# Performance work log

Measured on AMD Instinct MI355X. Metric: run time of the kernel, lower is better.

## Reference

```python
import jax, jax.numpy as jnp
import numpy as np

TOP_K = 32
NUM_RBF = 16
D_MIN, D_MAX = 2.0, 22.0
MAX_REL = 32  # max_relative_feature

# atom index order: N=0, Ca=1, C=2, O=3, Cb=4
# 24 (query, neighbor) atom pairs, in the exact order of the torch RBF_all list
_PA = np.array([0,2,3,4,1,1,1,1,0,0,0,4,4,3,0,2,3,4,2,3,4,2,3,2])
_PB = np.array([0,2,3,4,0,2,3,4,2,3,4,2,3,2,1,1,1,1,0,0,0,4,4,3])


def setup_inputs() -> dict:
    key = jax.random.key(0)
    ks = jax.random.split(key, 6)
    B, L = 4, 2048
    X = jax.random.normal(ks[0], (B, L, 4, 3), jnp.float32) * 3.0  # coords, ~protein scale
    mask = jnp.ones((B, L), jnp.float32)
    residue_idx = jnp.tile(jnp.arange(L, dtype=jnp.int32)[None, :], (B, 1))
    chain_labels = jax.random.randint(ks[1], (B, L), 0, 4)
    W_pos = jax.random.normal(ks[2], (2 * MAX_REL + 2, 16), jnp.float32) * 0.1  # [66,16]
    b_pos = jnp.zeros((16,), jnp.float32)
    W_edge = jax.random.normal(ks[3], (16 + 25 * NUM_RBF, 128), jnp.float32) * 0.05  # [416,128]
    ln_gamma = jnp.ones((128,), jnp.float32)
    ln_beta = jnp.zeros((128,), jnp.float32)
    return dict(X=X, mask=mask, residue_idx=residue_idx, chain_labels=chain_labels,
                W_pos=W_pos, b_pos=b_pos, W_edge=W_edge, ln_gamma=ln_gamma, ln_beta=ln_beta)


def _rbf(D):
    mu = jnp.linspace(D_MIN, D_MAX, NUM_RBF)
    sigma = (D_MAX - D_MIN) / NUM_RBF
    return jnp.exp(-(((D[..., None] - mu) / sigma) ** 2))


def reference(X, mask, residue_idx, chain_labels, W_pos, b_pos, W_edge, ln_gamma, ln_beta):
    B, L = X.shape[0], X.shape[1]
    N, Ca, C, O = X[:, :, 0], X[:, :, 1], X[:, :, 2], X[:, :, 3]
    b = Ca - N
    c = C - Ca
    a = jnp.cross(b, c)
    Cb = -0.58273431 * a + 0.56802827 * b - 0.54067466 * c + Ca

    # kNN graph on Ca distances (masked)
    m2 = mask[:, None, :] * mask[:, :, None]                      # [B,L,L]
    dX = Ca[:, None, :, :] - Ca[:, :, None, :]
    D = m2 * jnp.sqrt(jnp.sum(dX * dX, -1) + 1e-6)                # [B,L,L]
    D_max = jnp.max(D, -1, keepdims=True)
    D_adjust = D + (1.0 - m2) * D_max
    neg_vals, E_idx = jax.lax.top_k(-D_adjust, TOP_K)             # smallest-k
    D_neighbors = -neg_vals                                       # [B,L,K]

    atoms = jnp.stack([N, Ca, C, O, Cb], 0)                       # [5,B,L,3]
    bidx = jnp.arange(B)[:, None, None]
    nbr = atoms[:, bidx, E_idx]                                   # [5,B,L,K,3] gathered neighbor coords

    # 24 cross-atom RBFs (gather-then-distance == distance-then-gather)
    Aq = atoms[_PA]                                               # [24,B,L,3]
    Nk = nbr[_PB]                                                 # [24,B,L,K,3]
    Dp = jnp.sqrt(jnp.sum((Aq[:, :, :, None, :] - Nk) ** 2, -1) + 1e-6)  # [24,B,L,K]
    R0 = _rbf(D_neighbors)                                        # [B,L,K,16] (Ca-Ca)
    Rp = jnp.moveaxis(_rbf(Dp), 0, 3).reshape(B, L, TOP_K, 24 * NUM_RBF)
    RBF_all = jnp.concatenate([R0, Rp], -1)                       # [B,L,K,400]

    # positional / chain encodings
    ridx_nbr = residue_idx[bidx, E_idx]                           # [B,L,K]
    offset = residue_idx[:, :, None] - ridx_nbr
    ch_nbr = chain_labels[bidx, E_idx]
    E_chains = (chain_labels[:, :, None] == ch_nbr).astype(jnp.int32)
    d = jnp.clip(offset + MAX_REL, 0, 2 * MAX_REL) * E_chains + (1 - E_chains) * (2 * MAX_REL + 1)
    E_pos = W_pos[d] + b_pos                                      # one-hot @ W == row gather

    E = jnp.concatenate([E_pos, RBF_all], -1) @ W_edge            # [B,L,K,128]
    mu = E.mean(-1, keepdims=True)
    var = E.var(-1, keepdims=True)
    E = (E - mu) / jnp.sqrt(var + 1e-5) * ln_gamma + ln_beta
    return E, E_idx
```

## Files before the change

kernel.cpp:

```cpp
#include <hip/hip_runtime.h>
#include <stdint.h>

typedef _Float16 v8h __attribute__((ext_vector_type(8)));
typedef _Float16 v4h __attribute__((ext_vector_type(4)));
typedef float v4f __attribute__((ext_vector_type(4)));

#define BB 4
#define LL 2048
#define TOPK 32
#define NF 416
#define NOUT 128
#define NBINS 4096
#define NCAND 128
#define FBS 232

__device__ __constant__ int c_PA[24] = {0,2,3,4,1,1,1,1,0,0,0,4,4,3,0,2,3,4,2,3,4,2,3,2};
__device__ __constant__ int c_PB[24] = {0,2,3,4,0,2,3,4,2,3,4,2,3,2,1,1,1,1,0,0,0,4,4,3};

#define OFF_ATOMS 0u
#define OFF_CA    524288u
#define OFF_WT    655360u

static __device__ inline float dist_np(float4 a, float4 b) {
#pragma clang fp contract(off)
  float dx = a.x - b.x, dy = a.y - b.y, dz = a.z - b.z;
  float s = ((dx * dx + dy * dy) + dz * dz) + 1e-6f;
  return sqrtf(s);
}

static __device__ inline unsigned long long umin64(unsigned long long a, unsigned long long b) {
  return a < b ? a : b;
}
static __device__ inline unsigned long long umax64(unsigned long long a, unsigned long long b) {
  return a > b ? a : b;
}

static __device__ inline void rbf16(float d, _Float16* dst) {
  v8h h0, h1;
#pragma unroll
  for (int m = 0; m < 16; ++m) {
    float mu = 2.0f + (20.0f / 15.0f) * (float)m;
    float a = (d - mu) * 0.8f;
    float v = __expf(-a * a);
    if (m < 8) h0[m] = (_Float16)v;
    else h1[m - 8] = (_Float16)v;
  }
  *(v8h*)dst = h0;
  *(v8h*)(dst + 8) = h1;
}

static __device__ inline float pdist(const float* qa, const float* nb, int pp) {
  int ia = c_PA[pp] * 3, ib = c_PB[pp] * 3;
  float dx = qa[ia] - nb[ib];
  float dy = qa[ia + 1] - nb[ib + 1];
  float dz = qa[ia + 2] - nb[ib + 2];
  return sqrtf(dx * dx + dy * dy + dz * dz + 1e-6f);
}

__global__ __launch_bounds__(256) void prep_kernel(const float* __restrict__ X,
                                                   const float* __restrict__ W_edge,
                                                   float4* __restrict__ atomsP,
                                                   float4* __restrict__ CaP,
                                                   _Float16* __restrict__ Wt) {
  int idx = blockIdx.x * 256 + threadIdx.x;
  if (idx < BB * LL) {
    const float* xp = X + (size_t)idx * 12;
    float Nx = xp[0], Ny = xp[1], Nz = xp[2];
    float Cax = xp[3], Cay = xp[4], Caz = xp[5];
    float Cx = xp[6], Cy = xp[7], Cz = xp[8];
    float Ox = xp[9], Oy = xp[10], Oz = xp[11];
    float bx = Cax - Nx, by = Cay - Ny, bz = Caz - Nz;
    float cx = Cx - Cax, cy = Cy - Cay, cz = Cz - Caz;
    float ax = by * cz - bz * cy;
    float ay = bz * cx - bx * cz;
    float az = bx * cy - by * cx;
    float Cbx = -0.58273431f * ax + 0.56802827f * bx - 0.54067466f * cx + Cax;
    float Cby = -0.58273431f * ay + 0.56802827f * by - 0.54067466f * cy + Cay;
    float Cbz = -0.58273431f * az + 0.56802827f * bz - 0.54067466f * cz + Caz;
    atomsP[(size_t)idx * 4 + 0] = make_float4(Nx, Ny, Nz, Cax);
    atomsP[(size_t)idx * 4 + 1] = make_float4(Cay, Caz, Cx, Cy);
    atomsP[(size_t)idx * 4 + 2] = make_float4(Cz, Ox, Oy, Oz);
    atomsP[(size_t)idx * 4 + 3] = make_float4(Cbx, Cby, Cbz, 0.f);
    CaP[idx] = make_float4(Cax, Cay, Caz, 0.f);
  } else {
    int t = idx - BB * LL;
    if (t < NOUT * NF) {
      int n = t / NF;
      int k = t - n * NF;
      Wt[t] = (_Float16)W_edge[(size_t)k * NOUT + n];
    }
  }
}

__global__ __launch_bounds__(256) void topk_kernel(const float4* __restrict__ CaP,
                                                   float* __restrict__ outIdx) {
  __shared__ int hist[NBINS];
  __shared__ unsigned long long cand[NCAND];
  __shared__ int cnt;
  __shared__ int cb_s;
  __shared__ int wtot[4];
  int bid = blockIdx.x;
  int b = bid >> 11;
  int i = bid & (LL - 1);
  int tid = threadIdx.x;
  int lane = tid & 63, wid = tid >> 6;

  for (int t = tid; t < NBINS; t += 256) hist[t] = 0;
  if (tid < NCAND) cand[tid] = ~0ull;
  if (tid == 0) cnt = 0;

  const float4* Cb_ = CaP + (size_t)b * LL;
  float4 ci = Cb_[i];
  unsigned long long key[8];
#pragma unroll
  for (int t = 0; t < 8; ++t) {
    int j = tid + (t << 8);
    float d = dist_np(ci, Cb_[j]);
    key[t] = ((unsigned long long)__float_as_uint(d) << 32) | (unsigned)j;
  }
  __syncthreads();
#pragma unroll
  for (int t = 0; t < 8; ++t) {
    atomicAdd(&hist[(int)(key[t] >> 51)], 1);
  }
  __syncthreads();

  int base_bin = tid * (NBINS / 256);
  int psum = 0;
#pragma unroll
  for (int t = 0; t < NBINS / 256; ++t) psum += hist[base_bin + t];
  int incl = psum;
#pragma unroll
  for (int off = 1; off < 64; off <<= 1) {
    int o = __shfl_up(incl, off);
    if (lane >= off) incl += o;
  }
  if (lane == 63) wtot[wid] = incl;
  __syncthreads();
  int wbase = 0;
  for (int w = 0; w < wid; ++w) wbase += wtot[w];
  int base = wbase + incl - psum;
  if (base < TOPK && base + psum >= TOPK) {
    int run = base;
    for (int t = 0; t < NBINS / 256; ++t) {
      int h = hist[base_bin + t];
      if (run < TOPK && run + h >= TOPK) { cb_s = base_bin + t; break; }
      run += h;
    }
  }
  __syncthreads();

  int cb = cb_s;
#pragma unroll
  for (int t = 0; t < 8; ++t) {
    if ((int)(key[t] >> 51) <= cb) {
      int slot = atomicAdd(&cnt, 1);
      if (slot < NCAND) cand[slot] = key[t];
    }
  }
  __syncthreads();

  if (wid == 0) {
    unsigned long long x = cand[lane];
    unsigned long long y = cand[lane + 64];
#pragma unroll
    for (int k = 2; k <= 128; k <<= 1) {
#pragma unroll
      for (int j = 64; j >= 1; j >>= 1) {
        if (j >= k) continue;
        if (j == 64) {
          unsigned long long mn = umin64(x, y), mx = umax64(x, y);
          x = mn; y = mx;
        } else {
          unsigned long long px = __shfl_xor(x, j);
          bool upx = ((lane & k) == 0);
          bool lowx = ((lane & j) == 0);
          x = (lowx == upx) ? umin64(x, px) : umax64(x, px);
          unsigned long long py = __shfl_xor(y, j);
          bool upy = (((lane + 64) & k) == 0);
          y = (lowx == upy) ? umin64(y, py) : umax64(y, py);
        }
      }
    }
    if (lane < TOPK) {
      int j = (int)(x & 0xffffffffull);
      outIdx[bid * TOPK + lane] = (float)j;
    }
  }
}

__global__ __launch_bounds__(512, 4) void edge_kernel(
    const float4* __restrict__ atomsP, const float4* __restrict__ CaP,
    const _Float16* __restrict__ Wt, const float* __restrict__ outIdxF,
    const int* __restrict__ ridx, const int* __restrict__ chain,
    const float* __restrict__ W_pos, const float* __restrict__ b_pos,
    const float* __restrict__ gamma, const float* __restrict__ beta,
    float* __restrict__ outE) {
  __shared__ __align__(16) _Float16 Fb[128][FBS];
  __shared__ float na_f[128][17];
  __shared__ float qa_f[4][16];
  __shared__ float dnbr_s[128];
  __shared__ int dpos_s[128];
  __shared__ int nidx_s[128];
  __shared__ float partS[128][5];
  __shared__ float partQ[128][5];
  __shared__ float2 mr[128];

  int bid = blockIdx.x;
  int b = bid >> 9;
  int tid = threadIdx.x;
  int g0 = bid * 4;

  if (tid < 128) {
    int r = tid >> 5;
    int j = (int)outIdxF[(size_t)bid * 128 + tid];
    nidx_s[tid] = j;
    dnbr_s[tid] = dist_np(CaP[g0 + r], CaP[(size_t)b * LL + j]);
    int ri = ridx[g0 + r], rj = ridx[b * LL + j];
    int off = ri - rj + 32;
    off = off < 0 ? 0 : (off > 64 ? 64 : off);
    dpos_s[tid] = (chain[g0 + r] == chain[b * LL + j]) ? off : 65;
  } else if (tid < 144) {
    int q16 = tid - 128;
    int r = q16 >> 2, q = q16 & 3;
    float4 v = atomsP[(size_t)(g0 + r) * 4 + q];
    qa_f[r][q * 4 + 0] = v.x; qa_f[r][q * 4 + 1] = v.y;
    qa_f[r][q * 4 + 2] = v.z; qa_f[r][q * 4 + 3] = v.w;
  }
  __syncthreads();

  int e = tid >> 2, g = tid & 3;
  int rr = e >> 5;
  {
    float4 v = atomsP[((size_t)b * LL + nidx_s[e]) * 4 + g];
    na_f[e][g * 4 + 0] = v.x; na_f[e][g * 4 + 1] = v.y;
    na_f[e][g * 4 + 2] = v.z; na_f[e][g * 4 + 3] = v.w;
  }

  {
    int dp = dpos_s[e];
    v4h hp;
#pragma unroll
    for (int t = 0; t < 4; ++t)
      hp[t] = (_Float16)(W_pos[dp * 16 + g * 4 + t] + b_pos[g * 4 + t]);
    *(v4h*)&Fb[e][g * 4] = hp;
  }
  for (int s = g; s < 13; s += 4) {
    float d;
    int col;
    if (s == 0) { d = dnbr_s[e]; col = 16; }
    else { int pp = s - 1; col = 32 + pp * 16; d = pdist(qa_f[rr], na_f[e], pp); }
    rbf16(d, &Fb[e][col]);
  }
  __syncthreads();

  int lane = tid & 63, wv = tid >> 6;
  int mt = wv & 1, nh = wv >> 1;
  int lm = lane & 15, lq = lane >> 4;
  const _Float16* bp0 = Wt + (size_t)(nh * 32 + lm) * NF + lq * 8;
  const _Float16* bp1 = bp0 + 16 * NF;
  v4f acc[4][2];
#pragma unroll
  for (int t = 0; t < 4; ++t) { acc[t][0] = (v4f){0,0,0,0}; acc[t][1] = (v4f){0,0,0,0}; }

#pragma unroll
  for (int kk = 0; kk < 7; ++kk) {
    int k = kk * 32;
    v8h B0 = *(const v8h*)(bp0 + k);
    v8h B1 = *(const v8h*)(bp1 + k);
#pragma unroll
    for (int t = 0; t < 4; ++t) {
      v8h A = *(const v8h*)&Fb[mt * 64 + t * 16 + lm][lq * 8 + k];
      acc[t][0] = __builtin_amdgcn_mfma_f32_16x16x32_f16(A, B0, acc[t][0], 0, 0, 0);
      acc[t][1] = __builtin_amdgcn_mfma_f32_16x16x32_f16(A, B1, acc[t][1], 0, 0, 0);
    }
  }
  __syncthreads();

  for (int s = g; s < 12; s += 4) {
    int pp = 12 + s;
    float d = pdist(qa_f[rr], na_f[e], pp);
    rbf16(d, &Fb[e][s * 16]);
  }
  __syncthreads();

#pragma unroll
  for (int kk = 0; kk < 6; ++kk) {
    int k = kk * 32;
    v8h B0 = *(const v8h*)(bp0 + 224 + k);
    v8h B1 = *(const v8h*)(bp1 + 224 + k);
#pragma unroll
    for (int t = 0; t < 4; ++t) {
      v8h A = *(const v8h*)&Fb[mt * 64 + t * 16 + lm][lq * 8 + k];
      acc[t][0] = __builtin_amdgcn_mfma_f32_16x16x32_f16(A, B0, acc[t][0], 0, 0, 0);
      acc[t][1] = __builtin_amdgcn_mfma_f32_16x16x32_f16(A, B1, acc[t][1], 0, 0, 0);
    }
  }

#pragma unroll
  for (int t = 0; t < 4; ++t) {
#pragma unroll
    for (int r = 0; r < 4; ++r) {
      float s = acc[t][0][r] + acc[t][1][r];
      float q = acc[t][0][r] * acc[t][0][r] + acc[t][1][r] * acc[t][1][r];
#pragma unroll
      for (int off = 1; off <= 8; off <<= 1) {
        s += __shfl_xor(s, off);
        q += __shfl_xor(q, off);
      }
      if (lm == 0) {
        int row = mt * 64 + t * 16 + lq * 4 + r;
        partS[row][nh] = s;
        partQ[row][nh] = q;
      }
    }
  }
  __syncthreads();
  if (tid < 128) {
    float S = (partS[tid][0] + partS[tid][1]) + (partS[tid][2] + partS[tid][3]);
    float Q = (partQ[tid][0] + partQ[tid][1]) + (partQ[tid][2] + partQ[tid][3]);
    float mean = S * (1.0f / 128.0f);
    float var = Q * (1.0f / 128.0f) - mean * mean;
    mr[tid] = make_float2(mean, 1.0f / sqrtf(var + 1e-5f));
  }
  __syncthreads();
  float gm0 = gamma[nh * 32 + lm], gm1 = gamma[nh * 32 + 16 + lm];
  float bt0 = beta[nh * 32 + lm], bt1 = beta[nh * 32 + 16 + lm];
  float* op = outE + (size_t)bid * 128 * NOUT + nh * 32 + lm;
#pragma unroll
  for (int t = 0; t < 4; ++t) {
#pragma unroll
    for (int r = 0; r < 4; ++r) {
      int row = mt * 64 + t * 16 + lq * 4 + r;
      float2 m = mr[row];
      float* p = op + (size_t)row * NOUT;
      p[0]  = (acc[t][0][r] - m.x) * m.y * gm0 + bt0;
      p[16] = (acc[t][1][r] - m.x) * m.y * gm1 + bt1;
    }
  }
}

extern "C" void kernel_launch(void* const* d_in, const int* in_sizes, int n_in,
                              void* d_out, int out_size, void* d_ws, size_t ws_size,
                              hipStream_t stream) {
  const float* X = (const float*)d_in[0];
  const int* ridx = (const int*)d_in[2];
  const int* chain = (const int*)d_in[3];
  const float* W_pos = (const float*)d_in[4];
  const float* b_pos = (const float*)d_in[5];
  const float* W_edge = (const float*)d_in[6];
  const float* gamma = (const float*)d_in[7];
  const float* beta = (const float*)d_in[8];

  float* outE = (float*)d_out;
  float* outIdx = outE + (size_t)BB * LL * TOPK * NOUT;

  char* ws = (char*)d_ws;
  float4* atomsP = (float4*)(ws + OFF_ATOMS);
  float4* CaP = (float4*)(ws + OFF_CA);
  _Float16* Wt = (_Float16*)(ws + OFF_WT);

  prep_kernel<<<240, 256, 0, stream>>>(X, W_edge, atomsP, CaP, Wt);
  topk_kernel<<<BB * LL, 256, 0, stream>>>(CaP, outIdx);
  edge_kernel<<<BB * LL / 4, 512, 0, stream>>>(atomsP, CaP, Wt, outIdx, ridx, chain,
                                               W_pos, b_pos, gamma, beta, outE);
}
```

Before: 243.3 us.

## Use one wave per row in top-k and shrink edge kernel LDS for occupancy

The top-k kernel now assigns one wavefront per query row, with a 512-bin histogram over a clamped float-exponent range. Distances are recomputed in a second pass instead of being held as keys in registers, which removes block-wide syncs and cuts LDS per row. The edge kernel splits the feature staging into three smaller K chunks (128/128/160) so the shared feature buffer shrinks. It also aliases scratch arrays and raises the launch bound to 6 blocks per CU. The cost is more syncs, recomputed distances, and reliance on the clamped histogram range holding enough candidates.

New measurement: 259.5 us. +6.7%, slower.

```diff
diff --git a/kernel.cpp b/kernel.cpp
--- a/kernel.cpp
+++ b/kernel.cpp
@@ -10,9 +10,10 @@
 #define TOPK 32
 #define NF 416
 #define NOUT 128
-#define NBINS 4096
 #define NCAND 128
-#define FBS 232
+#define HBINS 512
+#define HLO 1792
+#define FBS2 168
 
 __device__ __constant__ int c_PA[24] = {0,2,3,4,1,1,1,1,0,0,0,4,4,3,0,2,3,4,2,3,4,2,3,2};
 __device__ __constant__ int c_PB[24] = {0,2,3,4,0,2,3,4,2,3,4,2,3,2,1,1,1,1,0,0,0,4,4,3};
@@ -49,11 +50,8 @@
   *(v8h*)(dst + 8) = h1;
 }
 
-static __device__ inline float pdist(const float* qa, const float* nb, int pp) {
-  int ia = c_PA[pp] * 3, ib = c_PB[pp] * 3;
-  float dx = qa[ia] - nb[ib];
-  float dy = qa[ia + 1] - nb[ib + 1];
-  float dz = qa[ia + 2] - nb[ib + 2];
+static __device__ inline float dist3(const float* a, const float* b) {
+  float dx = a[0] - b[0], dy = a[1] - b[1], dz = a[2] - b[2];
   return sqrtf(dx * dx + dy * dy + dz * dz + 1e-6f);
 }
 
@@ -94,75 +92,74 @@
 
 __global__ __launch_bounds__(256) void topk_kernel(const float4* __restrict__ CaP,
                                                    float* __restrict__ outIdx) {
-  __shared__ int hist[NBINS];
-  __shared__ unsigned long long cand[NCAND];
-  __shared__ int cnt;
-  __shared__ int cb_s;
-  __shared__ int wtot[4];
+  __shared__ int hist[4][HBINS];
+  __shared__ unsigned long long cand[4][NCAND];
+  __shared__ int cnt[4];
+  __shared__ int cbs[4];
+  int tid = threadIdx.x;
+  int lane = tid & 63, w = tid >> 6;
   int bid = blockIdx.x;
-  int b = bid >> 11;
-  int i = bid & (LL - 1);
-  int tid = threadIdx.x;
-  int lane = tid & 63, wid = tid >> 6;
-
-  for (int t = tid; t < NBINS; t += 256) hist[t] = 0;
-  if (tid < NCAND) cand[tid] = ~0ull;
-  if (tid == 0) cnt = 0;
-
+  int row = bid * 4 + w;
+  int b = row >> 11;
+  int i = row & (LL - 1);
   const float4* Cb_ = CaP + (size_t)b * LL;
+
+  for (int t = lane; t < HBINS; t += 64) hist[w][t] = 0;
+  cand[w][lane] = ~0ull;
+  cand[w][lane + 64] = ~0ull;
+  if (lane == 0) cnt[w] = 0;
   float4 ci = Cb_[i];
-  unsigned long long key[8];
-#pragma unroll
-  for (int t = 0; t < 8; ++t) {
-    int j = tid + (t << 8);
+  __syncthreads();
+
+  for (int t = 0; t < 32; ++t) {
+    int j = (t << 6) | lane;
     float d = dist_np(ci, Cb_[j]);
-    key[t] = ((unsigned long long)__float_as_uint(d) << 32) | (unsigned)j;
-  }
-  __syncthreads();
-#pragma unroll
-  for (int t = 0; t < 8; ++t) {
-    atomicAdd(&hist[(int)(key[t] >> 51)], 1);
-  }
-  __syncthreads();
-
-  int base_bin = tid * (NBINS / 256);
-  int psum = 0;
-#pragma unroll
-  for (int t = 0; t < NBINS / 256; ++t) psum += hist[base_bin + t];
-  int incl = psum;
-#pragma unroll
-  for (int off = 1; off < 64; off <<= 1) {
-    int o = __shfl_up(incl, off);
-    if (lane >= off) incl += o;
-  }
-  if (lane == 63) wtot[wid] = incl;
-  __syncthreads();
-  int wbase = 0;
-  for (int w = 0; w < wid; ++w) wbase += wtot[w];
-  int base = wbase + incl - psum;
-  if (base < TOPK && base + psum >= TOPK) {
-    int run = base;
-    for (int t = 0; t < NBINS / 256; ++t) {
-      int h = hist[base_bin + t];
-      if (run < TOPK && run + h >= TOPK) { cb_s = base_bin + t; break; }
-      run += h;
-    }
-  }
-  __syncthreads();
-
-  int cb = cb_s;
-#pragma unroll
-  for (int t = 0; t < 8; ++t) {
-    if ((int)(key[t] >> 51) <= cb) {
-      int slot = atomicAdd(&cnt, 1);
-      if (slot < NCAND) cand[slot] = key[t];
-    }
-  }
-  __syncthreads();
-
-  if (wid == 0) {
-    unsigned long long x = cand[lane];
-    unsigned long long y = cand[lane + 64];
+    int bin = (int)(__float_as_uint(d) >> 19) - HLO;
+    bin = bin < 0 ? 0 : (bin > HBINS - 1 ? HBINS - 1 : bin);
+    atomicAdd(&hist[w][bin], 1);
+  }
+  __syncthreads();
+
+  {
+    int base = lane * 8;
+    int h[8], psum = 0;
+#pragma unroll
+    for (int t = 0; t < 8; ++t) { h[t] = hist[w][base + t]; psum += h[t]; }
+    int incl = psum;
+#pragma unroll
+    for (int off = 1; off < 64; off <<= 1) {
+      int o = __shfl_up(incl, off);
+      if (lane >= off) incl += o;
+    }
+    int excl = incl - psum;
+    if (excl < TOPK && incl >= TOPK) {
+      int run = excl;
+#pragma unroll
+      for (int t = 0; t < 8; ++t) {
+        if (run < TOPK && run + h[t] >= TOPK) { cbs[w] = base + t; break; }
+        run += h[t];
+      }
+    }
+  }
+  __syncthreads();
+  int cb = cbs[w];
+
+  for (int t = 0; t < 32; ++t) {
+    int j = (t << 6) | lane;
+    float d = dist_np(ci, Cb_[j]);
+    int bin = (int)(__float_as_uint(d) >> 19) - HLO;
+    bin = bin < 0 ? 0 : (bin > HBINS - 1 ? HBINS - 1 : bin);
+    if (bin <= cb) {
+      int slot = atomicAdd(&cnt[w], 1);
+      if (slot < NCAND)
+        cand[w][slot] = ((unsigned long long)__float_as_uint(d) << 32) | (unsigned)j;
+    }
+  }
+  __syncthreads();
+
+  {
+    unsigned long long x = cand[w][lane];
+    unsigned long long y = cand[w][lane + 64];
 #pragma unroll
     for (int k = 2; k <= 128; k <<= 1) {
 #pragma unroll
@@ -184,27 +181,27 @@
     }
     if (lane < TOPK) {
       int j = (int)(x & 0xffffffffull);
-      outIdx[bid * TOPK + lane] = (float)j;
-    }
-  }
-}
-
-__global__ __launch_bounds__(512, 4) void edge_kernel(
-    const float4* __restrict__ atomsP, const float4* __restrict__ CaP,
+      outIdx[(size_t)row * TOPK + lane] = (float)j;
+    }
+  }
+}
+
+__global__ __launch_bounds__(512, 6) void edge_kernel(
+    const float4* __restrict__ atomsP,
     const _Float16* __restrict__ Wt, const float* __restrict__ outIdxF,
     const int* __restrict__ ridx, const int* __restrict__ chain,
     const float* __restrict__ W_pos, const float* __restrict__ b_pos,
     const float* __restrict__ gamma, const float* __restrict__ beta,
     float* __restrict__ outE) {
-  __shared__ __align__(16) _Float16 Fb[128][FBS];
-  __shared__ float na_f[128][17];
+  __shared__ __align__(16) _Float16 Fb[128][FBS2];
+  __shared__ __align__(16) char scratch[8704];
   __shared__ float qa_f[4][16];
-  __shared__ float dnbr_s[128];
   __shared__ int dpos_s[128];
   __shared__ int nidx_s[128];
-  __shared__ float partS[128][5];
-  __shared__ float partQ[128][5];
-  __shared__ float2 mr[128];
+  float (*na_f)[17] = (float (*)[17])scratch;
+  float (*partS)[5] = (float (*)[5])scratch;
+  float (*partQ)[5] = (float (*)[5])(scratch + 2560);
+  float2* mr = (float2*)(scratch + 5120);
 
   int bid = blockIdx.x;
   int b = bid >> 9;
@@ -215,7 +212,6 @@
     int r = tid >> 5;
     int j = (int)outIdxF[(size_t)bid * 128 + tid];
     nidx_s[tid] = j;
-    dnbr_s[tid] = dist_np(CaP[g0 + r], CaP[(size_t)b * LL + j]);
     int ri = ridx[g0 + r], rj = ridx[b * LL + j];
     int off = ri - rj + 32;
     off = off < 0 ? 0 : (off > 64 ? 64 : off);
@@ -237,6 +233,16 @@
     na_f[e][g * 4 + 2] = v.z; na_f[e][g * 4 + 3] = v.w;
   }
 
+  auto pdist = [&](int ee, int pp) -> float {
+    int ia = c_PA[pp] * 3, ib = c_PB[pp] * 3;
+    const float* qa = qa_f[rr];
+    const float* nb = na_f[ee];
+    float dx = qa[ia] - nb[ib];
+    float dy = qa[ia + 1] - nb[ib + 1];
+    float dz = qa[ia + 2] - nb[ib + 2];
+    return sqrtf(dx * dx + dy * dy + dz * dz + 1e-6f);
+  };
+
   {
     int dp = dpos_s[e];
     v4h hp;
@@ -245,12 +251,10 @@
       hp[t] = (_Float16)(W_pos[dp * 16 + g * 4 + t] + b_pos[g * 4 + t]);
     *(v4h*)&Fb[e][g * 4] = hp;
   }
-  for (int s = g; s < 13; s += 4) {
-    float d;
-    int col;
-    if (s == 0) { d = dnbr_s[e]; col = 16; }
-    else { int pp = s - 1; col = 32 + pp * 16; d = pdist(qa_f[rr], na_f[e], pp); }
-    rbf16(d, &Fb[e][col]);
+  for (int s = g; s < 7; s += 4) {
+    float d = (s == 0) ? dist3(&qa_f[rr][3], &na_f[e][3])
+                       : pdist(e, s - 1);
+    rbf16(d, &Fb[e][16 + s * 16]);
   }
   __syncthreads();
 
@@ -264,7 +268,7 @@
   for (int t = 0; t < 4; ++t) { acc[t][0] = (v4f){0,0,0,0}; acc[t][1] = (v4f){0,0,0,0}; }
 
 #pragma unroll
-  for (int kk = 0; kk < 7; ++kk) {
+  for (int kk = 0; kk < 4; ++kk) {
     int k = kk * 32;
     v8h B0 = *(const v8h*)(bp0 + k);
     v8h B1 = *(const v8h*)(bp1 + k);
@@ -277,18 +281,35 @@
   }
   __syncthreads();
 
-  for (int s = g; s < 12; s += 4) {
-    int pp = 12 + s;
-    float d = pdist(qa_f[rr], na_f[e], pp);
-    rbf16(d, &Fb[e][s * 16]);
-  }
-  __syncthreads();
-
-#pragma unroll
-  for (int kk = 0; kk < 6; ++kk) {
+  for (int s = g; s < 8; s += 4) {
+    rbf16(pdist(e, 6 + s), &Fb[e][s * 16]);
+  }
+  __syncthreads();
+
+#pragma unroll
+  for (int kk = 0; kk < 4; ++kk) {
     int k = kk * 32;
-    v8h B0 = *(const v8h*)(bp0 + 224 + k);
-    v8h B1 = *(const v8h*)(bp1 + 224 + k);
+    v8h B0 = *(const v8h*)(bp0 + 128 + k);
+    v8h B1 = *(const v8h*)(bp1 + 128 + k);
+#pragma unroll
+    for (int t = 0; t < 4; ++t) {
+      v8h A = *(const v8h*)&Fb[mt * 64 + t * 16 + lm][lq * 8 + k];
+      acc[t][0] = __builtin_amdgcn_mfma_f32_16x16x32_f16(A, B0, acc[t][0], 0, 0, 0);
+      acc[t][1] = __builtin_amdgcn_mfma_f32_16x16x32_f16(A, B1, acc[t][1], 0, 0, 0);
+    }
+  }
+  __syncthreads();
+
+  for (int s = g; s < 10; s += 4) {
+    rbf16(pdist(e, 14 + s), &Fb[e][s * 16]);
+  }
+  __syncthreads();
+
+#pragma unroll
+  for (int kk = 0; kk < 5; ++kk) {
+    int k = kk * 32;
+    v8h B0 = *(const v8h*)(bp0 + 256 + k);
+    v8h B1 = *(const v8h*)(bp1 + 256 + k);
 #pragma unroll
     for (int t = 0; t < 4; ++t) {
       v8h A = *(const v8h*)&Fb[mt * 64 + t * 16 + lm][lq * 8 + k];
@@ -361,7 +382,7 @@
   _Float16* Wt = (_Float16*)(ws + OFF_WT);
 
   prep_kernel<<<240, 256, 0, stream>>>(X, W_edge, atomsP, CaP, Wt);
-  topk_kernel<<<BB * LL, 256, 0, stream>>>(CaP, outIdx);
-  edge_kernel<<<BB * LL / 4, 512, 0, stream>>>(atomsP, CaP, Wt, outIdx, ridx, chain,
+  topk_kernel<<<BB * LL / 4, 256, 0, stream>>>(CaP, outIdx);
+  edge_kernel<<<BB * LL / 4, 512, 0, stream>>>(atomsP, Wt, outIdx, ridx, chain,
                                                W_pos, b_pos, gamma, beta, outE);
 }
```
